# Kernel optimization log

Hardware: AMD Instinct MI355X
Metric: run time of the kernel (lower is better)

The kernel has to match this reference:

```python
import jax, jax.numpy as jnp
import numpy as np

NUM_NODES = 100000
NUM_EDGES = 1600000
NUM_GRAPHS = 512
HIDDEN = 128
LAYERS = 3
NUM_CLASSES = 10
BN_EPS = 1e-5


def setup_inputs() -> dict:
    key = jax.random.key(0)
    ks = jax.random.split(key, 12)
    x = jax.random.normal(ks[0], (NUM_NODES, HIDDEN), dtype=jnp.float32)
    edge_index = jax.random.randint(ks[1], (2, NUM_EDGES), 0, NUM_NODES, dtype=jnp.int32)
    batch = jnp.sort(jax.random.randint(ks[2], (NUM_NODES,), 0, NUM_GRAPHS, dtype=jnp.int32))
    s = 1.0 / np.sqrt(HIDDEN)
    W1 = jax.random.normal(ks[3], (LAYERS, HIDDEN, HIDDEN), dtype=jnp.float32) * s
    b1 = jnp.zeros((LAYERS, HIDDEN), dtype=jnp.float32)
    W2 = jax.random.normal(ks[4], (LAYERS, HIDDEN, HIDDEN), dtype=jnp.float32) * s
    b2 = jnp.zeros((LAYERS, HIDDEN), dtype=jnp.float32)
    gamma = jnp.ones((LAYERS, HIDDEN), dtype=jnp.float32)
    beta = jnp.zeros((LAYERS, HIDDEN), dtype=jnp.float32)
    eps_gin = jnp.zeros((LAYERS,), dtype=jnp.float32)  # train_eps init 0
    lin1_w = jax.random.normal(ks[5], (LAYERS * HIDDEN, HIDDEN), dtype=jnp.float32) * (1.0 / np.sqrt(LAYERS * HIDDEN))
    lin1_b = jnp.zeros((HIDDEN,), dtype=jnp.float32)
    lin2_w = jax.random.normal(ks[6], (HIDDEN, NUM_CLASSES), dtype=jnp.float32) * s
    lin2_b = jnp.zeros((NUM_CLASSES,), dtype=jnp.float32)
    return {"x": x, "edge_index": edge_index, "batch": batch,
            "W1": W1, "b1": b1, "W2": W2, "b2": b2,
            "gamma": gamma, "beta": beta, "eps_gin": eps_gin,
            "lin1_w": lin1_w, "lin1_b": lin1_b, "lin2_w": lin2_w, "lin2_b": lin2_b}


def _batchnorm(h, g, b):
    mu = jnp.mean(h, axis=0, keepdims=True)
    var = jnp.var(h, axis=0, keepdims=True)
    return (h - mu) * jax.lax.rsqrt(var + BN_EPS) * g + b


def reference(x, edge_index, batch, W1, b1, W2, b2, gamma, beta, eps_gin,
              lin1_w, lin1_b, lin2_w, lin2_b):
    src, dst = edge_index[0], edge_index[1]
    n = x.shape[0]
    h = x
    layer_hs = []
    for l in range(LAYERS):
        # scatter-add neighbor aggregation: agg[i] = sum_{j->i} h[j]
        agg = jax.ops.segment_sum(h[src], dst, num_segments=n)
        z = (1.0 + eps_gin[l]) * h + agg
        z = jax.nn.relu(z @ W1[l] + b1[l])
        z = jax.nn.relu(z @ W2[l] + b2[l])
        h = _batchnorm(z, gamma[l], beta[l])
        layer_hs.append(h)
    h_cat = jnp.concatenate(layer_hs, axis=-1)  # [N, LAYERS*HIDDEN]
    # global mean pool per graph
    sums = jax.ops.segment_sum(h_cat, batch, num_segments=NUM_GRAPHS)
    counts = jax.ops.segment_sum(jnp.ones((n, 1), h_cat.dtype), batch, num_segments=NUM_GRAPHS)
    g = sums / jnp.maximum(counts, 1.0)
    g = jax.nn.relu(g @ lin1_w + lin1_b)
    # dropout is identity in inference
    return g @ lin2_w + lin2_b
```

## Files before the change

kernel.cpp:

```cpp
#include <hip/hip_runtime.h>

#define HID 128
#define NGRAPH 512
#define NLAYERS 3
#define BN_EPS 1e-5f
#define NPB 256
#define EB 4096

typedef __attribute__((ext_vector_type(8))) short bf16x8;
typedef __attribute__((ext_vector_type(4))) float f32x4;
typedef __attribute__((ext_vector_type(2))) float f32x2;

__device__ inline unsigned short f2bf(float x) {
    union { float f; unsigned u; } v; v.f = x;
    unsigned r = v.u + 0x7FFFu + ((v.u >> 16) & 1u);
    return (unsigned short)(r >> 16);
}
__device__ inline float bf2f(unsigned short b) {
    union { float f; unsigned u; } v; v.u = ((unsigned)b) << 16; return v.f;
}
__device__ inline f32x2 bfp(unsigned u) {
    union { unsigned q; float f; } lo, hi;
    lo.q = u << 16; hi.q = u & 0xFFFF0000u;
    f32x2 r; r[0] = lo.f; r[1] = hi.f; return r;
}

__global__ void k_prep(const float4* __restrict__ x4, ushort* __restrict__ xb, int total4,
                       const float* __restrict__ W1, ushort* __restrict__ w1h, ushort* __restrict__ w1l,
                       const float* __restrict__ W2, ushort* __restrict__ w2h, ushort* __restrict__ w2l,
                       int wtotal, int xblocks,
                       const int* __restrict__ dst, int E, int* __restrict__ blkcnt,
                       int* __restrict__ btot,
                       const int* __restrict__ batch, int N, int eblk, int* __restrict__ gcnt) {
    __shared__ int hist[512];
    int b = blockIdx.x, t = threadIdx.x;
    if (b < 384) {
        int gid = b * 256 + t;
        const float* W; ushort *Wh, *Wl; int e;
        if (gid < wtotal) { W = W1; Wh = w1h; Wl = w1l; e = gid; }
        else              { W = W2; Wh = w2h; Wl = w2l; e = gid - wtotal; }
        if (e < wtotal) {
            int l = e >> 14, rem = e & 16383, k = rem >> 7, n = rem & 127;
            float v = W[e];
            ushort hi = f2bf(v);
            ushort lo = f2bf(v - bf2f(hi));
            int o = (l << 14) + (n << 7) + k;
            Wh[o] = hi; Wl[o] = lo;
        }
    } else if (b < 384 + xblocks) {
        int i = (b - 384) * 256 + t;
        if (i < total4) {
            float4 v = x4[i];
            uint2 p;
            p.x = ((unsigned)f2bf(v.y) << 16) | f2bf(v.x);
            p.y = ((unsigned)f2bf(v.w) << 16) | f2bf(v.z);
            ((uint2*)xb)[i] = p;
        }
    } else if (b < 384 + xblocks + eblk) {
        int b2 = b - (384 + xblocks);
        hist[t] = 0; hist[t + 256] = 0;
        __syncthreads();
        int base = b2 * EB;
        #pragma unroll
        for (int i = 0; i < 16; ++i) {
            int e = base + i * 256 + t;
            if (e < E) atomicAdd(&hist[dst[e] >> 8], 1);
        }
        __syncthreads();
        blkcnt[b2 * 512 + t]       = hist[t];
        blkcnt[b2 * 512 + t + 256] = hist[t + 256];
        if (hist[t])       atomicAdd(&btot[t], hist[t]);
        if (hist[t + 256]) atomicAdd(&btot[t + 256], hist[t + 256]);
    } else {
        int b3 = b - (384 + xblocks + eblk);
        hist[t] = 0; hist[t + 256] = 0;
        __syncthreads();
        int base = b3 * 4096;
        #pragma unroll
        for (int i = 0; i < 16; ++i) {
            int n = base + i * 256 + t;
            if (n < N) atomicAdd(&hist[batch[n]], 1);
        }
        __syncthreads();
        if (hist[t])       atomicAdd(&gcnt[t], hist[t]);
        if (hist[t + 256]) atomicAdd(&gcnt[t + 256], hist[t + 256]);
    }
}

__global__ __launch_bounds__(512) void k_bscan(const int* __restrict__ tot, int nb, int E,
                                               int* __restrict__ bbase, int* __restrict__ rowptrN) {
    __shared__ int sh[512];
    int t = threadIdx.x;
    sh[t] = (t < nb) ? tot[t] : 0;
    __syncthreads();
    #pragma unroll
    for (int s = 1; s < 512; s <<= 1) {
        int v = (t >= s) ? sh[t - s] : 0;
        __syncthreads();
        sh[t] += v;
        __syncthreads();
    }
    if (t < nb) bbase[t] = (t == 0) ? 0 : sh[t - 1];
    if (t == 0) { bbase[nb] = E; *rowptrN = E; }
}

__global__ __launch_bounds__(512) void k_colscan(int* __restrict__ blkcnt, int eblk,
                                                 const int* __restrict__ bbase) {
    __shared__ int sh[512];
    int t = threadIdx.x;
    int b = blockIdx.x;
    sh[t] = (t < eblk) ? blkcnt[t * 512 + b] : 0;
    __syncthreads();
    #pragma unroll
    for (int s = 1; s < 512; s <<= 1) {
        int v = (t >= s) ? sh[t - s] : 0;
        __syncthreads();
        sh[t] += v;
        __syncthreads();
    }
    int excl = (t == 0) ? 0 : sh[t - 1];
    if (t < eblk) blkcnt[t * 512 + b] = bbase[b] + excl;
}

__global__ __launch_bounds__(256) void k_bscatter(const int* __restrict__ src,
                                                  const int* __restrict__ dst, int E,
                                                  const int* __restrict__ blkcnt,
                                                  unsigned* __restrict__ pairs) {
    __shared__ int hist[512];
    __shared__ int lbase[512];
    int t = threadIdx.x;
    hist[t] = 0; hist[t + 256] = 0;
    lbase[t]       = blkcnt[blockIdx.x * 512 + t];
    lbase[t + 256] = blkcnt[blockIdx.x * 512 + t + 256];
    __syncthreads();
    int base = blockIdx.x * EB;
    #pragma unroll
    for (int i = 0; i < 16; ++i) {
        int e = base + i * 256 + t;
        if (e < E) {
            int d = dst[e];
            int b = d >> 8;
            int pos = lbase[b] + atomicAdd(&hist[b], 1);
            pairs[pos] = ((unsigned)(d & 255) << 24) | (unsigned)src[e];
        }
    }
}

__global__ __launch_bounds__(256) void k_bbuild(const unsigned* __restrict__ pairs,
                                                const int* __restrict__ bbase, int N,
                                                int* __restrict__ rowptr, int* __restrict__ csr) {
    __shared__ int cnt[256];
    __shared__ int off[256];
    int t = threadIdx.x;
    int b = blockIdx.x;
    int base = bbase[b], bcount = bbase[b + 1] - base;
    cnt[t] = 0;
    __syncthreads();
    for (int i = t; i < bcount; i += 256) atomicAdd(&cnt[pairs[base + i] >> 24], 1);
    __syncthreads();
    off[t] = cnt[t];
    __syncthreads();
    for (int s = 1; s < 256; s <<= 1) {
        int v = (t >= s) ? off[t - s] : 0;
        __syncthreads();
        off[t] += v;
        __syncthreads();
    }
    int excl = (t == 0) ? 0 : off[t - 1];
    int node = b * NPB + t;
    if (node < N) rowptr[node] = base + excl;
    cnt[t] = excl;
    __syncthreads();
    for (int i = t; i < bcount; i += 256) {
        unsigned p = pairs[base + i];
        int dl = p >> 24;
        int pos = base + atomicAdd(&cnt[dl], 1);
        csr[pos] = (int)(p & 0xFFFFFFu);
    }
}

__global__ __launch_bounds__(256, 6) void k_agg(
        const int* __restrict__ rowptr, const int* __restrict__ csr_src,
        const uint2* __restrict__ hinb,
        const float* __restrict__ prev_sliced,
        const float* __restrict__ g_row, const float* __restrict__ be_row,
        const float* __restrict__ eps_gin, int layer,
        ushort* __restrict__ z0out, int N) {
    __shared__ float sfold[256];
    const int t = threadIdx.x;
    const int lane = t & 63;
    const int wv = t >> 6;
    const int q = lane >> 4;
    const int f = lane & 15;

    if (prev_sliced) {
        float s = 0.f;
        #pragma unroll
        for (int k = 0; k < 8; ++k) s += prev_sliced[k * 768 + t];
        sfold[t] = s;
        __syncthreads();
    }

    f32x2 scv2[4], shv2[4];
    if (prev_sliced) {
        float invn = 1.0f / (float)N;
        #pragma unroll
        for (int d = 0; d < 4; ++d) {
            #pragma unroll
            for (int h = 0; h < 2; ++h) {
                int fi = f * 8 + d * 2 + h;
                float mu = sfold[fi] * invn;
                float var = sfold[128 + fi] * invn - mu * mu;
                float inv = rsqrtf(var + BN_EPS);
                float scj = g_row[fi] * inv;
                scv2[d][h] = scj; shv2[d][h] = be_row[fi] - mu * scj;
            }
        }
    } else {
        #pragma unroll
        for (int d = 0; d < 4; ++d) { scv2[d] = (f32x2){1.f, 1.f}; shv2[d] = (f32x2){0.f, 0.f}; }
    }
    float e1 = 1.0f + eps_gin[layer];
    const uint4* hin4 = (const uint4*)hinb;

    int r = blockIdx.x * 16 + wv * 4 + q;
    f32x2 a2[4];
    #pragma unroll
    for (int d = 0; d < 4; ++d) a2[d] = (f32x2){0.f, 0.f};
    float cdeg = 0.f;
    if (r < N) {
        int beg = rowptr[r], end = rowptr[r + 1];
        uint4 hv = hin4[(size_t)r * 16 + f];
        a2[0] = e1 * bfp(hv.x); a2[1] = e1 * bfp(hv.y);
        a2[2] = e1 * bfp(hv.z); a2[3] = e1 * bfp(hv.w);
        int p = beg;
        for (; p + 8 <= end; p += 8) {
            int s0 = csr_src[p],     s1 = csr_src[p + 1], s2 = csr_src[p + 2], s3 = csr_src[p + 3];
            int s4 = csr_src[p + 4], s5 = csr_src[p + 5], s6 = csr_src[p + 6], s7 = csr_src[p + 7];
            uint4 v0 = hin4[(size_t)s0 * 16 + f];
            uint4 v1 = hin4[(size_t)s1 * 16 + f];
            uint4 v2 = hin4[(size_t)s2 * 16 + f];
            uint4 v3 = hin4[(size_t)s3 * 16 + f];
            uint4 v4 = hin4[(size_t)s4 * 16 + f];
            uint4 v5 = hin4[(size_t)s5 * 16 + f];
            uint4 v6 = hin4[(size_t)s6 * 16 + f];
            uint4 v7 = hin4[(size_t)s7 * 16 + f];
            a2[0] += ((bfp(v0.x) + bfp(v1.x)) + (bfp(v2.x) + bfp(v3.x)))
                   + ((bfp(v4.x) + bfp(v5.x)) + (bfp(v6.x) + bfp(v7.x)));
            a2[1] += ((bfp(v0.y) + bfp(v1.y)) + (bfp(v2.y) + bfp(v3.y)))
                   + ((bfp(v4.y) + bfp(v5.y)) + (bfp(v6.y) + bfp(v7.y)));
            a2[2] += ((bfp(v0.z) + bfp(v1.z)) + (bfp(v2.z) + bfp(v3.z)))
                   + ((bfp(v4.z) + bfp(v5.z)) + (bfp(v6.z) + bfp(v7.z)));
            a2[3] += ((bfp(v0.w) + bfp(v1.w)) + (bfp(v2.w) + bfp(v3.w)))
                   + ((bfp(v4.w) + bfp(v5.w)) + (bfp(v6.w) + bfp(v7.w)));
        }
        if (p < end) {
            int last = end - 1;
            int c1 = min(p + 1, last), c2 = min(p + 2, last), c3 = min(p + 3, last);
            int c4 = min(p + 4, last), c5 = min(p + 5, last), c6 = min(p + 6, last);
            int s0 = csr_src[p],  s1 = csr_src[c1], s2 = csr_src[c2], s3 = csr_src[c3];
            int s4 = csr_src[c4], s5 = csr_src[c5], s6 = csr_src[c6];
            uint4 v0 = hin4[(size_t)s0 * 16 + f];
            uint4 v1 = hin4[(size_t)s1 * 16 + f];
            uint4 v2 = hin4[(size_t)s2 * 16 + f];
            uint4 v3 = hin4[(size_t)s3 * 16 + f];
            uint4 v4 = hin4[(size_t)s4 * 16 + f];
            uint4 v5 = hin4[(size_t)s5 * 16 + f];
            uint4 v6 = hin4[(size_t)s6 * 16 + f];
            int rem = end - p;
            unsigned m1 = (rem > 1) ? 0xFFFFFFFFu : 0u;
            unsigned m2 = (rem > 2) ? 0xFFFFFFFFu : 0u;
            unsigned m3 = (rem > 3) ? 0xFFFFFFFFu : 0u;
            unsigned m4 = (rem > 4) ? 0xFFFFFFFFu : 0u;
            unsigned m5 = (rem > 5) ? 0xFFFFFFFFu : 0u;
            unsigned m6 = (rem > 6) ? 0xFFFFFFFFu : 0u;
            a2[0] += ((bfp(v0.x) + bfp(v1.x & m1)) + (bfp(v2.x & m2) + bfp(v3.x & m3)))
                   + ((bfp(v4.x & m4) + bfp(v5.x & m5)) + bfp(v6.x & m6));
            a2[1] += ((bfp(v0.y) + bfp(v1.y & m1)) + (bfp(v2.y & m2) + bfp(v3.y & m3)))
                   + ((bfp(v4.y & m4) + bfp(v5.y & m5)) + bfp(v6.y & m6));
            a2[2] += ((bfp(v0.z) + bfp(v1.z & m1)) + (bfp(v2.z & m2) + bfp(v3.z & m3)))
                   + ((bfp(v4.z & m4) + bfp(v5.z & m5)) + bfp(v6.z & m6));
            a2[3] += ((bfp(v0.w) + bfp(v1.w & m1)) + (bfp(v2.w & m2) + bfp(v3.w & m3)))
                   + ((bfp(v4.w & m4) + bfp(v5.w & m5)) + bfp(v6.w & m6));
        }
        cdeg = e1 + (float)(end - beg);
    }
    f32x2 rr2[4];
    #pragma unroll
    for (int d = 0; d < 4; ++d) rr2[d] = scv2[d] * a2[d] + cdeg * shv2[d];
    uint4 ph;
    ph.x = ((unsigned)f2bf(rr2[0][1]) << 16) | f2bf(rr2[0][0]);
    ph.y = ((unsigned)f2bf(rr2[1][1]) << 16) | f2bf(rr2[1][0]);
    ph.z = ((unsigned)f2bf(rr2[2][1]) << 16) | f2bf(rr2[2][0]);
    ph.w = ((unsigned)f2bf(rr2[3][1]) << 16) | f2bf(rr2[3][0]);
    if (r < N) ((uint4*)z0out)[(size_t)r * 16 + f] = ph;
}

__global__ __launch_bounds__(256, 2) void k_mlp_dense(
        const uint4* __restrict__ z0, int layer, const int* __restrict__ batch,
        const ushort* __restrict__ w1h, const ushort* __restrict__ w1l,
        const float* __restrict__ b1,
        const ushort* __restrict__ w2h, const ushort* __restrict__ w2l,
        const float* __restrict__ b2,
        ushort* __restrict__ Hout, float* __restrict__ stat_sl,
        float* __restrict__ gsum, int N) {
    __shared__ __align__(16) ushort smem[8192];
    const int t = threadIdx.x;
    const int lane = t & 63;
    const int wv = t >> 6;
    const int li = lane & 15;
    const int kq = lane >> 4;
    const int n0 = wv * 32;
    const int row0 = blockIdx.x * 64;
    const int swz = (li & 7) * 4;

    bf16x8 w1hr[8], w1lr[8], w2hr[8], w2lr[8];
    #pragma unroll
    for (int ch = 0; ch < 2; ++ch)
        #pragma unroll
        for (int ks = 0; ks < 2; ++ks)
            #pragma unroll
            for (int nt = 0; nt < 2; ++nt) {
                int i = ch * 4 + ks * 2 + nt;
                size_t wo = (size_t)(n0 + nt * 16 + li) * 128 + (ch * 64 + ks * 32 + kq * 8);
                w1hr[i] = *(const bf16x8*)&w1h[wo];
                w1lr[i] = *(const bf16x8*)&w1l[wo];
                w2hr[i] = *(const bf16x8*)&w2h[wo];
                w2lr[i] = *(const bf16x8*)&w2l[wo];
            }

    {
        const uint4 zz = {0u, 0u, 0u, 0u};
        #pragma unroll
        for (int i = 0; i < 4; ++i) {
            int idx = i * 256 + t;
            int r = idx >> 4, f = idx & 15;
            uint4 v = (row0 + r < N) ? z0[(size_t)(row0 + r) * 16 + f] : zz;
            ((uint4*)smem)[r * 16 + (f ^ (r & 7))] = v;
        }
    }
    __syncthreads();

    f32x4 acc[4][2];
    #pragma unroll
    for (int i = 0; i < 4; ++i) {
        acc[i][0] = (f32x4){0.f, 0.f, 0.f, 0.f};
        acc[i][1] = (f32x4){0.f, 0.f, 0.f, 0.f};
    }

    #pragma unroll
    for (int ch = 0; ch < 2; ++ch) {
        #pragma unroll
        for (int ks = 0; ks < 2; ++ks) {
            int kcol = ch * 8 + ks * 4 + kq;
            #pragma unroll
            for (int mt = 0; mt < 4; ++mt) {
                int r = mt * 16 + li;
                int hw = (r * 16 + (kcol ^ (li & 7))) * 8;
                bf16x8 ah = *(const bf16x8*)&smem[hw];
                #pragma unroll
                for (int nt = 0; nt < 2; ++nt) {
                    int i = ch * 4 + ks * 2 + nt;
                    acc[mt][nt] = __builtin_amdgcn_mfma_f32_16x16x32_bf16(ah, w1hr[i], acc[mt][nt], 0, 0, 0);
                    acc[mt][nt] = __builtin_amdgcn_mfma_f32_16x16x32_bf16(ah, w1lr[i], acc[mt][nt], 0, 0, 0);
                }
            }
        }
    }

    float bz0 = b1[n0 + li], bz1 = b1[n0 + 16 + li];
    __syncthreads();
    #pragma unroll
    for (int mt = 0; mt < 4; ++mt) {
        #pragma unroll
        for (int nt = 0; nt < 2; ++nt) {
            int c = n0 + nt * 16 + li;
            int dk = c >> 1;
            int halfbase = (dk >> 5) * 32;
            int dlow = dk & 31;
            int codd = c & 1;
            float bias = nt ? bz1 : bz0;
            #pragma unroll
            for (int reg = 0; reg < 4; ++reg) {
                int r = mt * 16 + kq * 4 + reg;
                float v = fmaxf(acc[mt][nt][reg] + bias, 0.f);
                int us = (r * 64 + halfbase + (dlow ^ ((r & 7) * 4))) * 2 + codd;
                smem[us] = f2bf(v);
            }
        }
    }
    #pragma unroll
    for (int i = 0; i < 4; ++i) {
        acc[i][0] = (f32x4){0.f, 0.f, 0.f, 0.f};
        acc[i][1] = (f32x4){0.f, 0.f, 0.f, 0.f};
    }
    __syncthreads();

    #pragma unroll
    for (int ch = 0; ch < 2; ++ch) {
        #pragma unroll
        for (int ks = 0; ks < 2; ++ks) {
            int aoff = (ks * 16 + kq * 4) ^ swz;
            #pragma unroll
            for (int mt = 0; mt < 4; ++mt) {
                int idx = ((mt * 16 + li) * 64 + ch * 32 + aoff) * 2;
                bf16x8 ah = *(const bf16x8*)&smem[idx];
                #pragma unroll
                for (int nt = 0; nt < 2; ++nt) {
                    int i = ch * 4 + ks * 2 + nt;
                    acc[mt][nt] = __builtin_amdgcn_mfma_f32_16x16x32_bf16(ah, w2hr[i], acc[mt][nt], 0, 0, 0);
                    acc[mt][nt] = __builtin_amdgcn_mfma_f32_16x16x32_bf16(ah, w2lr[i], acc[mt][nt], 0, 0, 0);
                }
            }
        }
    }

    float bb0 = b2[n0 + li], bb1 = b2[n0 + 16 + li];
    int btr[4][4];
    #pragma unroll
    for (int mt = 0; mt < 4; ++mt)
        #pragma unroll
        for (int reg = 0; reg < 4; ++reg) {
            int grow = row0 + mt * 16 + kq * 4 + reg;
            btr[mt][reg] = (grow < N) ? batch[grow] : -1;
        }
    __syncthreads();
    float s0 = 0.f, q0 = 0.f, s1 = 0.f, q1 = 0.f;
    #pragma unroll
    for (int mt = 0; mt < 4; ++mt) {
        #pragma unroll
        for (int reg = 0; reg < 4; ++reg) {
            int r = mt * 16 + kq * 4 + reg;
            float v0 = fmaxf(acc[mt][0][reg] + bb0, 0.f);
            float v1 = fmaxf(acc[mt][1][reg] + bb1, 0.f);
            smem[r * 128 + n0 + li]      = f2bf(v0);
            smem[r * 128 + n0 + 16 + li] = f2bf(v1);
            if (btr[mt][reg] >= 0) {
                s0 += v0; q0 += v0 * v0; s1 += v1; q1 += v1 * v1;
            }
        }
    }
    __syncthreads();
    {
        int valid = N - row0; if (valid > 64) valid = 64;
        int tot = valid * 16;
        for (int i = t; i < tot; i += 256) {
            int r = i >> 4, c = i & 15;
            ((uint4*)&Hout[(size_t)(row0 + r) * HID])[c] = ((const uint4*)smem)[r * 16 + c];
        }
    }
    s0 += __shfl_xor(s0, 16); s0 += __shfl_xor(s0, 32);
    q0 += __shfl_xor(q0, 16); q0 += __shfl_xor(q0, 32);
    s1 += __shfl_xor(s1, 16); s1 += __shfl_xor(s1, 32);
    q1 += __shfl_xor(q1, 16); q1 += __shfl_xor(q1, 32);
    if (kq == 0) {
        float* ss = stat_sl + (blockIdx.x & 7) * 768;
        unsafeAtomicAdd(&ss[n0 + li], s0);
        unsafeAtomicAdd(&ss[128 + n0 + li], q0);
        unsafeAtomicAdd(&ss[n0 + 16 + li], s1);
        unsafeAtomicAdd(&ss[128 + n0 + 16 + li], q1);
    }
    int lastr = N - 1; if (lastr > row0 + 63) lastr = row0 + 63;
    int g_lo = batch[row0], g_hi = batch[lastr];
    int loff = layer * HID;
    for (int g = g_lo; g <= g_hi; ++g) {
        float p0 = 0.f, p1 = 0.f;
        #pragma unroll
        for (int mt = 0; mt < 4; ++mt)
            #pragma unroll
            for (int reg = 0; reg < 4; ++reg) {
                if (btr[mt][reg] == g) {
                    p0 += fmaxf(acc[mt][0][reg] + bb0, 0.f);
                    p1 += fmaxf(acc[mt][1][reg] + bb1, 0.f);
                }
            }
        p0 += __shfl_xor(p0, 16); p0 += __shfl_xor(p0, 32);
        p1 += __shfl_xor(p1, 16); p1 += __shfl_xor(p1, 32);
        if (kq == 0) {
            unsafeAtomicAdd(&gsum[(size_t)g * 384 + loff + n0 + li], p0);
            unsafeAtomicAdd(&gsum[(size_t)g * 384 + loff + n0 + 16 + li], p1);
        }
    }
}

__global__ __launch_bounds__(256) void k_mlp(const int* __restrict__ gcnt, int N,
                     const float* __restrict__ gsum, const float* __restrict__ sliced,
                     const float* __restrict__ gamma, const float* __restrict__ beta,
                     const float* __restrict__ w1, const float* __restrict__ b1,
                     const float* __restrict__ w2, const float* __restrict__ b2,
                     float* __restrict__ out) {
    __shared__ float gl[384];
    __shared__ float ph[2][128];
    __shared__ float hh[128];
    int g = blockIdx.x, t = threadIdx.x;
    float cnt = (float)gcnt[g];
    float invc = 1.0f / fmaxf(cnt, 1.0f);
    float invn = 1.0f / (float)N;
    for (int i = t; i < 384; i += 256) {
        int l = i >> 7, f = i & 127;
        float sum_ = 0.f, sq_ = 0.f;
        #pragma unroll
        for (int k = 0; k < 8; ++k) {
            sum_ += sliced[k * 768 + l * 256 + f];
            sq_  += sliced[k * 768 + l * 256 + 128 + f];
        }
        float mu = sum_ * invn;
        float var = sq_ * invn - mu * mu;
        float inv = rsqrtf(var + BN_EPS);
        float sc = gamma[l * HID + f] * inv;
        float sh = beta[l * HID + f] - mu * sc;
        gl[i] = (gsum[(size_t)g * 384 + i] * sc + sh * cnt) * invc;
    }
    __syncthreads();
    int f = t & 127, kh = t >> 7;
    float acc = kh ? 0.f : b1[f];
    for (int k = kh * 192; k < kh * 192 + 192; ++k)
        acc = fmaf(gl[k], w1[k * HID + f], acc);
    ph[kh][f] = acc;
    __syncthreads();
    if (t < 128) hh[t] = fmaxf(ph[0][t] + ph[1][t], 0.f);
    __syncthreads();
    if (t < 64) {
        float h0 = hh[t], h1 = hh[t + 64];
        float p[10];
        #pragma unroll
        for (int o = 0; o < 10; ++o)
            p[o] = h0 * w2[t * 10 + o] + h1 * w2[(t + 64) * 10 + o];
        #pragma unroll
        for (int o = 0; o < 10; ++o) {
            #pragma unroll
            for (int s = 32; s > 0; s >>= 1) p[o] += __shfl_xor(p[o], s);
        }
        if (t == 0) {
            #pragma unroll
            for (int o = 0; o < 10; ++o) out[g * 10 + o] = b2[o] + p[o];
        }
    }
}

extern "C" void kernel_launch(void* const* d_in, const int* in_sizes, int n_in,
                              void* d_out, int out_size, void* d_ws, size_t ws_size,
                              hipStream_t stream) {
    const float* x     = (const float*)d_in[0];
    const int*   ei    = (const int*)d_in[1];
    const int*   batch = (const int*)d_in[2];
    const float* W1    = (const float*)d_in[3];
    const float* b1    = (const float*)d_in[4];
    const float* W2    = (const float*)d_in[5];
    const float* b2    = (const float*)d_in[6];
    const float* gamma = (const float*)d_in[7];
    const float* beta  = (const float*)d_in[8];
    const float* epsg  = (const float*)d_in[9];
    const float* l1w   = (const float*)d_in[10];
    const float* l1b   = (const float*)d_in[11];
    const float* l2w   = (const float*)d_in[12];
    const float* l2b   = (const float*)d_in[13];

    const int N = in_sizes[0] / HID;
    const int E = in_sizes[1] / 2;
    const int* src = ei;
    const int* dst = ei + E;
    const int nb = (N + NPB - 1) / NPB;
    const int eblk = (E + EB - 1) / EB;

    float* w = (float*)d_ws;
    const size_t NF = (size_t)N * HID;
    ushort* xb    = (ushort*)(w + NF);
    ushort* hb[3] = { xb + NF, xb + 2 * NF, xb + 3 * NF };
    ushort* z0buf = xb + 4 * NF;
    float* sliced = w + 4 * NF;
    float* gsum   = sliced + 6144;
    int*   btot   = (int*)(gsum + (size_t)NGRAPH * 384);
    int*   gcnt   = btot + 513;
    int*   rowptr = gcnt + 512;
    int*   csr    = rowptr + N + 1;
    int*   bbase  = csr + E;
    ushort* wt  = (ushort*)(((uintptr_t)(bbase + nb + 2) + 15) & ~(uintptr_t)15);
    ushort* w1h = wt;
    ushort* w1l = wt + 49152;
    ushort* w2h = wt + 98304;
    ushort* w2l = wt + 147456;

    unsigned* pairs  = (unsigned*)w;
    int*      blkcnt = (int*)(w + 2 * 1024 * 1024);

    hipMemsetAsync(sliced, 0, (6144 + (size_t)NGRAPH * 384 + 513 + 512) * sizeof(float), stream);

    const int total4 = (int)(NF / 4);
    const int xblocks = (total4 + 255) / 256;
    const int gblocks = (N + 4095) / 4096;
    const int prep_blocks = 384 + xblocks + eblk + gblocks;
    k_prep<<<prep_blocks, 256, 0, stream>>>((const float4*)x, xb, total4,
                                            W1, w1h, w1l, W2, w2h, w2l, NLAYERS * HID * HID,
                                            xblocks, dst, E, blkcnt, btot,
                                            batch, N, eblk, gcnt);

    k_bscan<<<1, 512, 0, stream>>>(btot, nb, E, bbase, rowptr + N);
    k_colscan<<<nb, 512, 0, stream>>>(blkcnt, eblk, bbase);
    k_bscatter<<<eblk, 256, 0, stream>>>(src, dst, E, blkcnt, pairs);
    k_bbuild<<<nb, 256, 0, stream>>>(pairs, bbase, N, rowptr, csr);

    for (int l = 0; l < NLAYERS; ++l) {
        const ushort* hin = (l == 0) ? xb : hb[l - 1];
        const float* psl    = (l == 0) ? nullptr : (sliced + (l - 1) * 256);
        const float* grow_  = gamma + (l == 0 ? 0 : (l - 1)) * HID;
        const float* brow_  = beta  + (l == 0 ? 0 : (l - 1)) * HID;

        k_agg<<<(N + 15) / 16, 256, 0, stream>>>(
            rowptr, csr, (const uint2*)hin, psl, grow_, brow_, epsg, l, z0buf, N);

        k_mlp_dense<<<(N + 63) / 64, 256, 0, stream>>>(
            (const uint4*)z0buf, l, batch,
            w1h + (size_t)l * 16384, w1l + (size_t)l * 16384, b1 + l * HID,
            w2h + (size_t)l * 16384, w2l + (size_t)l * 16384, b2 + l * HID,
            hb[l], sliced + l * 256, gsum, N);
    }

    k_mlp<<<NGRAPH, 256, 0, stream>>>(gcnt, N, gsum, sliced, gamma, beta,
                                      l1w, l1b, l2w, l2b, (float*)d_out);
}
```

Before: 517.6 us.

## Make dense MLP kernel persistent and merge bucket scan into column scan

The dense MLP kernel now runs a fixed 512-block grid that loops over 64-row tiles. Each block loads its split-bf16 weight registers and biases once and reuses them across tiles, instead of reloading them in every one of about 1563 blocks. Separately, the single-block bucket scan is folded into the column-scan kernel, where each block redundantly scans the bucket totals, which saves one launch. The trade-off is reduced latency hiding, since there are fewer resident blocks, plus an extra barrier per tile and redundant scan work per block.

```diff
diff --git a/kernel.cpp b/kernel.cpp
--- a/kernel.cpp
+++ b/kernel.cpp
@@ -87,11 +87,14 @@
     }
 }
 
-__global__ __launch_bounds__(512) void k_bscan(const int* __restrict__ tot, int nb, int E,
-                                               int* __restrict__ bbase, int* __restrict__ rowptrN) {
+__global__ __launch_bounds__(512) void k_colscan(int* __restrict__ blkcnt, int eblk,
+                                                 const int* __restrict__ btot, int nb, int E,
+                                                 int* __restrict__ bbase, int* __restrict__ rowptrN) {
     __shared__ int sh[512];
+    __shared__ int bb;
     int t = threadIdx.x;
-    sh[t] = (t < nb) ? tot[t] : 0;
+    int b = blockIdx.x;
+    sh[t] = (t < nb) ? btot[t] : 0;
     __syncthreads();
     #pragma unroll
     for (int s = 1; s < 512; s <<= 1) {
@@ -100,15 +103,12 @@
         sh[t] += v;
         __syncthreads();
     }
-    if (t < nb) bbase[t] = (t == 0) ? 0 : sh[t - 1];
-    if (t == 0) { bbase[nb] = E; *rowptrN = E; }
-}
-
-__global__ __launch_bounds__(512) void k_colscan(int* __restrict__ blkcnt, int eblk,
-                                                 const int* __restrict__ bbase) {
-    __shared__ int sh[512];
-    int t = threadIdx.x;
-    int b = blockIdx.x;
+    if (t == b) bb = (b == 0) ? 0 : sh[b - 1];
+    __syncthreads();
+    int base_b = bb;
+    if (t == 0) bbase[b] = base_b;
+    if (b == 0 && t == 0) { bbase[nb] = E; *rowptrN = E; }
+    __syncthreads();
     sh[t] = (t < eblk) ? blkcnt[t * 512 + b] : 0;
     __syncthreads();
     #pragma unroll
@@ -119,7 +119,7 @@
         __syncthreads();
     }
     int excl = (t == 0) ? 0 : sh[t - 1];
-    if (t < eblk) blkcnt[t * 512 + b] = bbase[b] + excl;
+    if (t < eblk) blkcnt[t * 512 + b] = base_b + excl;
 }
 
 __global__ __launch_bounds__(256) void k_bscatter(const int* __restrict__ src,
@@ -303,7 +303,7 @@
         const ushort* __restrict__ w2h, const ushort* __restrict__ w2l,
         const float* __restrict__ b2,
         ushort* __restrict__ Hout, float* __restrict__ stat_sl,
-        float* __restrict__ gsum, int N) {
+        float* __restrict__ gsum, int N, int ntiles) {
     __shared__ __align__(16) ushort smem[8192];
     const int t = threadIdx.x;
     const int lane = t & 63;
@@ -311,7 +311,6 @@
     const int li = lane & 15;
     const int kq = lane >> 4;
     const int n0 = wv * 32;
-    const int row0 = blockIdx.x * 64;
     const int swz = (li & 7) * 4;
 
     bf16x8 w1hr[8], w1lr[8], w2hr[8], w2lr[8];
@@ -328,158 +327,163 @@
                 w2hr[i] = *(const bf16x8*)&w2h[wo];
                 w2lr[i] = *(const bf16x8*)&w2l[wo];
             }
-
-    {
-        const uint4 zz = {0u, 0u, 0u, 0u};
+    float bz0 = b1[n0 + li], bz1 = b1[n0 + 16 + li];
+    float bb0 = b2[n0 + li], bb1 = b2[n0 + 16 + li];
+
+    for (int tile = blockIdx.x; tile < ntiles; tile += gridDim.x) {
+        const int row0 = tile * 64;
+
+        {
+            const uint4 zz = {0u, 0u, 0u, 0u};
+            #pragma unroll
+            for (int i = 0; i < 4; ++i) {
+                int idx = i * 256 + t;
+                int r = idx >> 4, f = idx & 15;
+                uint4 v = (row0 + r < N) ? z0[(size_t)(row0 + r) * 16 + f] : zz;
+                ((uint4*)smem)[r * 16 + (f ^ (r & 7))] = v;
+            }
+        }
+        __syncthreads();
+
+        f32x4 acc[4][2];
         #pragma unroll
         for (int i = 0; i < 4; ++i) {
-            int idx = i * 256 + t;
-            int r = idx >> 4, f = idx & 15;
-            uint4 v = (row0 + r < N) ? z0[(size_t)(row0 + r) * 16 + f] : zz;
-            ((uint4*)smem)[r * 16 + (f ^ (r & 7))] = v;
-        }
-    }
-    __syncthreads();
-
-    f32x4 acc[4][2];
-    #pragma unroll
-    for (int i = 0; i < 4; ++i) {
-        acc[i][0] = (f32x4){0.f, 0.f, 0.f, 0.f};
-        acc[i][1] = (f32x4){0.f, 0.f, 0.f, 0.f};
-    }
-
-    #pragma unroll
-    for (int ch = 0; ch < 2; ++ch) {
-        #pragma unroll
-        for (int ks = 0; ks < 2; ++ks) {
-            int kcol = ch * 8 + ks * 4 + kq;
-            #pragma unroll
-            for (int mt = 0; mt < 4; ++mt) {
-                int r = mt * 16 + li;
-                int hw = (r * 16 + (kcol ^ (li & 7))) * 8;
-                bf16x8 ah = *(const bf16x8*)&smem[hw];
+            acc[i][0] = (f32x4){0.f, 0.f, 0.f, 0.f};
+            acc[i][1] = (f32x4){0.f, 0.f, 0.f, 0.f};
+        }
+
+        #pragma unroll
+        for (int ch = 0; ch < 2; ++ch) {
+            #pragma unroll
+            for (int ks = 0; ks < 2; ++ks) {
+                int kcol = ch * 8 + ks * 4 + kq;
                 #pragma unroll
-                for (int nt = 0; nt < 2; ++nt) {
-                    int i = ch * 4 + ks * 2 + nt;
-                    acc[mt][nt] = __builtin_amdgcn_mfma_f32_16x16x32_bf16(ah, w1hr[i], acc[mt][nt], 0, 0, 0);
-                    acc[mt][nt] = __builtin_amdgcn_mfma_f32_16x16x32_bf16(ah, w1lr[i], acc[mt][nt], 0, 0, 0);
+                for (int mt = 0; mt < 4; ++mt) {
+                    int r = mt * 16 + li;
+                    int hw = (r * 16 + (kcol ^ (li & 7))) * 8;
+                    bf16x8 ah = *(const bf16x8*)&smem[hw];
+                    #pragma unroll
+                    for (int nt = 0; nt < 2; ++nt) {
+                        int i = ch * 4 + ks * 2 + nt;
+                        acc[mt][nt] = __builtin_amdgcn_mfma_f32_16x16x32_bf16(ah, w1hr[i], acc[mt][nt], 0, 0, 0);
+                        acc[mt][nt] = __builtin_amdgcn_mfma_f32_16x16x32_bf16(ah, w1lr[i], acc[mt][nt], 0, 0, 0);
+                    }
                 }
             }
         }
-    }
-
-    float bz0 = b1[n0 + li], bz1 = b1[n0 + 16 + li];
-    __syncthreads();
-    #pragma unroll
-    for (int mt = 0; mt < 4; ++mt) {
-        #pragma unroll
-        for (int nt = 0; nt < 2; ++nt) {
-            int c = n0 + nt * 16 + li;
-            int dk = c >> 1;
-            int halfbase = (dk >> 5) * 32;
-            int dlow = dk & 31;
-            int codd = c & 1;
-            float bias = nt ? bz1 : bz0;
+
+        __syncthreads();
+        #pragma unroll
+        for (int mt = 0; mt < 4; ++mt) {
+            #pragma unroll
+            for (int nt = 0; nt < 2; ++nt) {
+                int c = n0 + nt * 16 + li;
+                int dk = c >> 1;
+                int halfbase = (dk >> 5) * 32;
+                int dlow = dk & 31;
+                int codd = c & 1;
+                float bias = nt ? bz1 : bz0;
+                #pragma unroll
+                for (int reg = 0; reg < 4; ++reg) {
+                    int r = mt * 16 + kq * 4 + reg;
+                    float v = fmaxf(acc[mt][nt][reg] + bias, 0.f);
+                    int us = (r * 64 + halfbase + (dlow ^ ((r & 7) * 4))) * 2 + codd;
+                    smem[us] = f2bf(v);
+                }
+            }
+        }
+        #pragma unroll
+        for (int i = 0; i < 4; ++i) {
+            acc[i][0] = (f32x4){0.f, 0.f, 0.f, 0.f};
+            acc[i][1] = (f32x4){0.f, 0.f, 0.f, 0.f};
+        }
+        __syncthreads();
+
+        #pragma unroll
+        for (int ch = 0; ch < 2; ++ch) {
+            #pragma unroll
+            for (int ks = 0; ks < 2; ++ks) {
+                int aoff = (ks * 16 + kq * 4) ^ swz;
+                #pragma unroll
+                for (int mt = 0; mt < 4; ++mt) {
+                    int idx = ((mt * 16 + li) * 64 + ch * 32 + aoff) * 2;
+                    bf16x8 ah = *(const bf16x8*)&smem[idx];
+                    #pragma unroll
+                    for (int nt = 0; nt < 2; ++nt) {
+                        int i = ch * 4 + ks * 2 + nt;
+                        acc[mt][nt] = __builtin_amdgcn_mfma_f32_16x16x32_bf16(ah, w2hr[i], acc[mt][nt], 0, 0, 0);
+                        acc[mt][nt] = __builtin_amdgcn_mfma_f32_16x16x32_bf16(ah, w2lr[i], acc[mt][nt], 0, 0, 0);
+                    }
+                }
+            }
+        }
+
+        int btr[4][4];
+        #pragma unroll
+        for (int mt = 0; mt < 4; ++mt)
+            #pragma unroll
+            for (int reg = 0; reg < 4; ++reg) {
+                int grow = row0 + mt * 16 + kq * 4 + reg;
+                btr[mt][reg] = (grow < N) ? batch[grow] : -1;
+            }
+        __syncthreads();
+        float s0 = 0.f, q0 = 0.f, s1 = 0.f, q1 = 0.f;
+        #pragma unroll
+        for (int mt = 0; mt < 4; ++mt) {
             #pragma unroll
             for (int reg = 0; reg < 4; ++reg) {
                 int r = mt * 16 + kq * 4 + reg;
-                float v = fmaxf(acc[mt][nt][reg] + bias, 0.f);
-                int us = (r * 64 + halfbase + (dlow ^ ((r & 7) * 4))) * 2 + codd;
-                smem[us] = f2bf(v);
-            }
-        }
-    }
-    #pragma unroll
-    for (int i = 0; i < 4; ++i) {
-        acc[i][0] = (f32x4){0.f, 0.f, 0.f, 0.f};
-        acc[i][1] = (f32x4){0.f, 0.f, 0.f, 0.f};
-    }
-    __syncthreads();
-
-    #pragma unroll
-    for (int ch = 0; ch < 2; ++ch) {
-        #pragma unroll
-        for (int ks = 0; ks < 2; ++ks) {
-            int aoff = (ks * 16 + kq * 4) ^ swz;
-            #pragma unroll
-            for (int mt = 0; mt < 4; ++mt) {
-                int idx = ((mt * 16 + li) * 64 + ch * 32 + aoff) * 2;
-                bf16x8 ah = *(const bf16x8*)&smem[idx];
+                float v0 = fmaxf(acc[mt][0][reg] + bb0, 0.f);
+                float v1 = fmaxf(acc[mt][1][reg] + bb1, 0.f);
+                smem[r * 128 + n0 + li]      = f2bf(v0);
+                smem[r * 128 + n0 + 16 + li] = f2bf(v1);
+                if (btr[mt][reg] >= 0) {
+                    s0 += v0; q0 += v0 * v0; s1 += v1; q1 += v1 * v1;
+                }
+            }
+        }
+        __syncthreads();
+        {
+            int valid = N - row0; if (valid > 64) valid = 64;
+            int tot = valid * 16;
+            for (int i = t; i < tot; i += 256) {
+                int r = i >> 4, c = i & 15;
+                ((uint4*)&Hout[(size_t)(row0 + r) * HID])[c] = ((const uint4*)smem)[r * 16 + c];
+            }
+        }
+        s0 += __shfl_xor(s0, 16); s0 += __shfl_xor(s0, 32);
+        q0 += __shfl_xor(q0, 16); q0 += __shfl_xor(q0, 32);
+        s1 += __shfl_xor(s1, 16); s1 += __shfl_xor(s1, 32);
+        q1 += __shfl_xor(q1, 16); q1 += __shfl_xor(q1, 32);
+        if (kq == 0) {
+            float* ss = stat_sl + (blockIdx.x & 7) * 768;
+            unsafeAtomicAdd(&ss[n0 + li], s0);
+            unsafeAtomicAdd(&ss[128 + n0 + li], q0);
+            unsafeAtomicAdd(&ss[n0 + 16 + li], s1);
+            unsafeAtomicAdd(&ss[128 + n0 + 16 + li], q1);
+        }
+        int lastr = N - 1; if (lastr > row0 + 63) lastr = row0 + 63;
+        int g_lo = batch[row0], g_hi = batch[lastr];
+        int loff = layer * HID;
+        for (int g = g_lo; g <= g_hi; ++g) {
+            float p0 = 0.f, p1 = 0.f;
+            #pragma unroll
+            for (int mt = 0; mt < 4; ++mt)
                 #pragma unroll
-                for (int nt = 0; nt < 2; ++nt) {
-                    int i = ch * 4 + ks * 2 + nt;
-                    acc[mt][nt] = __builtin_amdgcn_mfma_f32_16x16x32_bf16(ah, w2hr[i], acc[mt][nt], 0, 0, 0);
-                    acc[mt][nt] = __builtin_amdgcn_mfma_f32_16x16x32_bf16(ah, w2lr[i], acc[mt][nt], 0, 0, 0);
+                for (int reg = 0; reg < 4; ++reg) {
+                    if (btr[mt][reg] == g) {
+                        p0 += fmaxf(acc[mt][0][reg] + bb0, 0.f);
+                        p1 += fmaxf(acc[mt][1][reg] + bb1, 0.f);
+                    }
                 }
-            }
-        }
-    }
-
-    float bb0 = b2[n0 + li], bb1 = b2[n0 + 16 + li];
-    int btr[4][4];
-    #pragma unroll
-    for (int mt = 0; mt < 4; ++mt)
-        #pragma unroll
-        for (int reg = 0; reg < 4; ++reg) {
-            int grow = row0 + mt * 16 + kq * 4 + reg;
-            btr[mt][reg] = (grow < N) ? batch[grow] : -1;
-        }
-    __syncthreads();
-    float s0 = 0.f, q0 = 0.f, s1 = 0.f, q1 = 0.f;
-    #pragma unroll
-    for (int mt = 0; mt < 4; ++mt) {
-        #pragma unroll
-        for (int reg = 0; reg < 4; ++reg) {
-            int r = mt * 16 + kq * 4 + reg;
-            float v0 = fmaxf(acc[mt][0][reg] + bb0, 0.f);
-            float v1 = fmaxf(acc[mt][1][reg] + bb1, 0.f);
-            smem[r * 128 + n0 + li]      = f2bf(v0);
-            smem[r * 128 + n0 + 16 + li] = f2bf(v1);
-            if (btr[mt][reg] >= 0) {
-                s0 += v0; q0 += v0 * v0; s1 += v1; q1 += v1 * v1;
-            }
-        }
-    }
-    __syncthreads();
-    {
-        int valid = N - row0; if (valid > 64) valid = 64;
-        int tot = valid * 16;
-        for (int i = t; i < tot; i += 256) {
-            int r = i >> 4, c = i & 15;
-            ((uint4*)&Hout[(size_t)(row0 + r) * HID])[c] = ((const uint4*)smem)[r * 16 + c];
-        }
-    }
-    s0 += __shfl_xor(s0, 16); s0 += __shfl_xor(s0, 32);
-    q0 += __shfl_xor(q0, 16); q0 += __shfl_xor(q0, 32);
-    s1 += __shfl_xor(s1, 16); s1 += __shfl_xor(s1, 32);
-    q1 += __shfl_xor(q1, 16); q1 += __shfl_xor(q1, 32);
-    if (kq == 0) {
-        float* ss = stat_sl + (blockIdx.x & 7) * 768;
-        unsafeAtomicAdd(&ss[n0 + li], s0);
-        unsafeAtomicAdd(&ss[128 + n0 + li], q0);
-        unsafeAtomicAdd(&ss[n0 + 16 + li], s1);
-        unsafeAtomicAdd(&ss[128 + n0 + 16 + li], q1);
-    }
-    int lastr = N - 1; if (lastr > row0 + 63) lastr = row0 + 63;
-    int g_lo = batch[row0], g_hi = batch[lastr];
-    int loff = layer * HID;
-    for (int g = g_lo; g <= g_hi; ++g) {
-        float p0 = 0.f, p1 = 0.f;
-        #pragma unroll
-        for (int mt = 0; mt < 4; ++mt)
-            #pragma unroll
-            for (int reg = 0; reg < 4; ++reg) {
-                if (btr[mt][reg] == g) {
-                    p0 += fmaxf(acc[mt][0][reg] + bb0, 0.f);
-                    p1 += fmaxf(acc[mt][1][reg] + bb1, 0.f);
-                }
-            }
-        p0 += __shfl_xor(p0, 16); p0 += __shfl_xor(p0, 32);
-        p1 += __shfl_xor(p1, 16); p1 += __shfl_xor(p1, 32);
-        if (kq == 0) {
-            unsafeAtomicAdd(&gsum[(size_t)g * 384 + loff + n0 + li], p0);
-            unsafeAtomicAdd(&gsum[(size_t)g * 384 + loff + n0 + 16 + li], p1);
-        }
+            p0 += __shfl_xor(p0, 16); p0 += __shfl_xor(p0, 32);
+            p1 += __shfl_xor(p1, 16); p1 += __shfl_xor(p1, 32);
+            if (kq == 0) {
+                unsafeAtomicAdd(&gsum[(size_t)g * 384 + loff + n0 + li], p0);
+                unsafeAtomicAdd(&gsum[(size_t)g * 384 + loff + n0 + 16 + li], p1);
+            }
+        }
+        __syncthreads();
     }
 }
 
@@ -595,11 +599,11 @@
                                             xblocks, dst, E, blkcnt, btot,
                                             batch, N, eblk, gcnt);
 
-    k_bscan<<<1, 512, 0, stream>>>(btot, nb, E, bbase, rowptr + N);
-    k_colscan<<<nb, 512, 0, stream>>>(blkcnt, eblk, bbase);
+    k_colscan<<<nb, 512, 0, stream>>>(blkcnt, eblk, btot, nb, E, bbase, rowptr + N);
     k_bscatter<<<eblk, 256, 0, stream>>>(src, dst, E, blkcnt, pairs);
     k_bbuild<<<nb, 256, 0, stream>>>(pairs, bbase, N, rowptr, csr);
 
+    const int ntiles = (N + 63) / 64;
     for (int l = 0; l < NLAYERS; ++l) {
         const ushort* hin = (l == 0) ? xb : hb[l - 1];
         const float* psl    = (l == 0) ? nullptr : (sliced + (l - 1) * 256);
@@ -609,11 +613,11 @@
         k_agg<<<(N + 15) / 16, 256, 0, stream>>>(
             rowptr, csr, (const uint2*)hin, psl, grow_, brow_, epsg, l, z0buf, N);
 
-        k_mlp_dense<<<(N + 63) / 64, 256, 0, stream>>>(
+        k_mlp_dense<<<512, 256, 0, stream>>>(
             (const uint4*)z0buf, l, batch,
             w1h + (size_t)l * 16384, w1l + (size_t)l * 16384, b1 + l * HID,
             w2h + (size_t)l * 16384, w2l + (size_t)l * 16384, b2 + l * HID,
-            hb[l], sliced + l * 256, gsum, N);
+            hb[l], sliced + l * 256, gsum, N, ntiles);
     }
 
     k_mlp<<<NGRAPH, 256, 0, stream>>>(gcnt, N, gsum, sliced, gamma, beta,
```

After: 489.1 us. -5.5%, faster.
